# Kernel optimization log

Measured on AMD Instinct MI355X. Metric: run time of the kernel, lower is better.

Reference implementation:

```python
import jax, jax.numpy as jnp
import numpy as np

N = 50000      # nodes
E = 400000     # edges
D = 128        # node / hidden dim
DE = 64        # edge feature dim
Z = 2 * D + DE # CGConv concat dim


def setup_inputs() -> dict:
    key = jax.random.key(0)
    ks = jax.random.split(key, 12)
    s = 0.05
    return {
        "x": jax.random.normal(ks[0], (N, D), jnp.float32),
        "edge_index": jax.random.randint(ks[1], (2, E), 0, N, jnp.int64),
        "edge_attr": jax.random.normal(ks[2], (E, DE), jnp.float32),
        # conv1 params (lin_f: gate, lin_s: core), z-dim -> D
        "Wf1": jax.random.normal(ks[3], (Z, D), jnp.float32) * s,
        "bf1": jnp.zeros((D,), jnp.float32),
        "Ws1": jax.random.normal(ks[4], (Z, D), jnp.float32) * s,
        "bs1": jnp.zeros((D,), jnp.float32),
        # conv2 params
        "Wf2": jax.random.normal(ks[5], (Z, D), jnp.float32) * s,
        "bf2": jnp.zeros((D,), jnp.float32),
        "Ws2": jax.random.normal(ks[6], (Z, D), jnp.float32) * s,
        "bs2": jnp.zeros((D,), jnp.float32),
        # final linear D -> 1
        "Wfc": jax.random.normal(ks[7], (D, 1), jnp.float32) * s,
        "bfc": jnp.zeros((1,), jnp.float32),
    }


def _cgconv(h, edge_attr, src, dst, Wf, bf, Ws, bs):
    # PyG CGConv: z_ij = [x_i, x_j, e_ij]; out_i = x_i + sum_j sigmoid(lin_f(z)) * softplus(lin_s(z))
    # x_i = target = edge_index[1], x_j = source = edge_index[0]
    z = jnp.concatenate([h[dst], h[src], edge_attr], axis=-1)  # [E, Z]
    msg = jax.nn.sigmoid(z @ Wf + bf) * jax.nn.softplus(z @ Ws + bs)  # [E, D]
    agg = jax.ops.segment_sum(msg, dst, num_segments=h.shape[0])  # [N, D]
    return h + agg


def reference(x, edge_index, edge_attr, Wf1, bf1, Ws1, bs1, Wf2, bf2, Ws2, bs2, Wfc, bfc):
    src, dst = edge_index[0], edge_index[1]
    h = _cgconv(x, edge_attr, src, dst, Wf1, bf1, Ws1, bs1)
    h = jax.nn.relu(h)
    h = _cgconv(h, edge_attr, src, dst, Wf2, bf2, Ws2, bs2)
    return h @ Wfc + bfc  # [N, 1]
```

## Files before the change

### kernel.cpp

```cpp
#include <hip/hip_runtime.h>
#include <math.h>

#define NN 50000
#define NE 400000

typedef __attribute__((ext_vector_type(8))) short bf16x8;
typedef __attribute__((ext_vector_type(4))) float f32x4;
typedef unsigned short ushort_t;

__device__ __forceinline__ unsigned short f2bf(float f) {
    unsigned int u = __float_as_uint(f);
    u += 0x7FFF + ((u >> 16) & 1);
    return (unsigned short)(u >> 16);
}
__device__ __forceinline__ float2 upk(unsigned int w) {
    float2 r;
    r.x = __uint_as_float(w << 16);
    r.y = __uint_as_float(w & 0xFFFF0000u);
    return r;
}

#define LOG2E 1.4426950408889634f
#define LN2   0.6931471805599453f

__device__ __forceinline__ float msg_act(float gf, float gs) {
    float tf = __builtin_amdgcn_exp2f(gf * -LOG2E);
    float sig = __builtin_amdgcn_rcpf(1.0f + tf) * LN2;
    float ts = __builtin_amdgcn_exp2f(gs * LOG2E);
    float lg = __builtin_amdgcn_logf(1.0f + ts);
    return sig * lg;
}

__global__ void pack_weights(const float* __restrict__ Wf, const float* __restrict__ bf,
                             const float* __restrict__ Ws, const float* __restrict__ bs,
                             ushort_t* __restrict__ WT, ushort_t* __restrict__ WeT,
                             float* __restrict__ bcat) {
    int i = blockIdx.x * 256 + threadIdx.x;
    if (i < 512 * 128) {
        int c = i >> 7, k = i & 127;
        float w;
        if (c < 128)      w = Wf[k * 128 + c];
        else if (c < 256) w = Wf[(128 + k) * 128 + (c - 128)];
        else if (c < 384) w = Ws[k * 128 + (c - 256)];
        else              w = Ws[(128 + k) * 128 + (c - 384)];
        WT[i] = f2bf(w);
    } else if (i < 512 * 128 + 256 * 64) {
        int j = i - 512 * 128;
        int c = j >> 6, k = j & 63;
        float w = (c < 128) ? Wf[(256 + k) * 128 + c] : Ws[(256 + k) * 128 + (c - 128)];
        WeT[j] = f2bf(w);
    } else if (i < 512 * 128 + 256 * 64 + 256) {
        int c = i - (512 * 128 + 256 * 64);
        bcat[c] = (c < 128) ? bf[c] : bs[c - 128];
    }
}

__global__ void cvt_bf16(const float* __restrict__ in, ushort_t* __restrict__ out, int n8) {
    int i = blockIdx.x * 256 + threadIdx.x;
    if (i >= n8) return;
    const float4* p = (const float4*)in + (size_t)i * 2;
    float4 a = p[0], b = p[1];
    bf16x8 v;
    v[0] = (short)f2bf(a.x); v[1] = (short)f2bf(a.y);
    v[2] = (short)f2bf(a.z); v[3] = (short)f2bf(a.w);
    v[4] = (short)f2bf(b.x); v[5] = (short)f2bf(b.y);
    v[6] = (short)f2bf(b.z); v[7] = (short)f2bf(b.w);
    *((bf16x8*)out + i) = v;
}

__global__ __launch_bounds__(256) void node_gemm(const ushort_t* __restrict__ hb,
                                                 const ushort_t* __restrict__ WT,
                                                 ushort_t* __restrict__ P) {
    __shared__ ushort_t Bs[128 * 136];
    const int tid = threadIdx.x;
    const int w = tid >> 6, l = tid & 63;
    const int by = blockIdx.y;
    const ushort_t* src = WT + (size_t)by * 128 * 128;
    #pragma unroll
    for (int j = 0; j < 8; ++j) {
        int cid = j * 256 + tid;
        int row = cid >> 4, off = (cid & 15) * 8;
        *(bf16x8*)(&Bs[row * 136 + off]) = *(const bf16x8*)(src + row * 128 + off);
    }
    __syncthreads();
    const int r0 = blockIdx.x * 64 + w * 16;
    const int lrow = l & 15, lk = l >> 4;
    int arow = r0 + lrow;
    if (arow >= NN) arow = NN - 1;
    f32x4 acc[8];
    #pragma unroll
    for (int i = 0; i < 8; ++i) acc[i] = (f32x4){0.f, 0.f, 0.f, 0.f};
    #pragma unroll
    for (int ks = 0; ks < 4; ++ks) {
        int kb = ks * 32 + lk * 8;
        bf16x8 af = *(const bf16x8*)(hb + (size_t)arow * 128 + kb);
        #pragma unroll
        for (int nc = 0; nc < 8; ++nc) {
            bf16x8 bfr = *(const bf16x8*)(&Bs[(nc * 16 + lrow) * 136 + kb]);
            acc[nc] = __builtin_amdgcn_mfma_f32_16x16x32_bf16(af, bfr, acc[nc], 0, 0, 0);
        }
    }
    const int rb = r0 + lk * 4;
    const int cb = by * 128;
    #pragma unroll
    for (int nc = 0; nc < 8; ++nc) {
        int col = cb + nc * 16 + lrow;
        #pragma unroll
        for (int r = 0; r < 4; ++r) {
            int row = rb + r;
            if (row < NN) P[(size_t)row * 512 + col] = f2bf(acc[nc][r]);
        }
    }
}

__global__ __launch_bounds__(512) void edge_fused(const int* __restrict__ ei,
                                                  const ushort_t* __restrict__ eab,
                                                  const ushort_t* __restrict__ WeT,
                                                  const float* __restrict__ bcat,
                                                  const ushort_t* __restrict__ P,
                                                  ushort_t* __restrict__ hacc) {
    __shared__ ushort_t Qs[64 * 264];
    const int tid = threadIdx.x;
    const int w = tid >> 6, l = tid & 63;
    const int lrow = l & 15, lk = l >> 4;
    const int e0 = blockIdx.x * 64;

    const int tile = w >> 1, half = w & 1;
    f32x4 acc[8];
    #pragma unroll
    for (int i = 0; i < 8; ++i) acc[i] = (f32x4){0.f, 0.f, 0.f, 0.f};
    const int arow = e0 + tile * 16 + lrow;
    const ushort_t* wslice = WeT + (size_t)half * 128 * 64;
    #pragma unroll
    for (int ks = 0; ks < 2; ++ks) {
        int kb = ks * 32 + lk * 8;
        bf16x8 af = *(const bf16x8*)(eab + (size_t)arow * 64 + kb);
        #pragma unroll
        for (int nc = 0; nc < 8; ++nc) {
            bf16x8 bfr = *(const bf16x8*)(wslice + (size_t)(nc * 16 + lrow) * 64 + kb);
            acc[nc] = __builtin_amdgcn_mfma_f32_16x16x32_bf16(af, bfr, acc[nc], 0, 0, 0);
        }
    }
    #pragma unroll
    for (int nc = 0; nc < 8; ++nc) {
        int col = half * 128 + nc * 16 + lrow;
        float bb = bcat[col];
        #pragma unroll
        for (int r = 0; r < 4; ++r) {
            Qs[(tile * 16 + lk * 4 + r) * 264 + col] = f2bf(acc[nc][r] + bb);
        }
    }
    __syncthreads();

    #pragma unroll
    for (int i = 0; i < 8; ++i) {
        int j = w * 8 + i;
        int e = e0 + j;
        int s = ei[e];
        int d = ei[NE + e];
        const unsigned int* Pd = (const unsigned int*)(P + (size_t)d * 512);
        const unsigned int* Ps = (const unsigned int*)(P + (size_t)s * 512);
        float2 af_ = upk(Pd[l]);
        float2 bf_ = upk(Ps[64 + l]);
        float2 as_ = upk(Pd[128 + l]);
        float2 bs_ = upk(Ps[192 + l]);
        const unsigned int* qr = (const unsigned int*)(Qs + (size_t)j * 264);
        float2 qf = upk(qr[l]);
        float2 qs = upk(qr[64 + l]);
        float m0 = msg_act(af_.x + bf_.x + qf.x, as_.x + bs_.x + qs.x);
        float m1 = msg_act(af_.y + bf_.y + qf.y, as_.y + bs_.y + qs.y);
        unsigned int pk = (unsigned int)f2bf(m0) | ((unsigned int)f2bf(m1) << 16);
        unsigned int* addr = (unsigned int*)(hacc + (size_t)d * 128 + 2 * l);
        asm volatile("global_atomic_pk_add_bf16 %0, %1, off" :: "v"(addr), "v"(pk));
    }
}

__global__ void relu_bf(const ushort_t* __restrict__ in, ushort_t* __restrict__ out, int n8) {
    int i = blockIdx.x * 256 + threadIdx.x;
    if (i >= n8) return;
    uint4 v = ((const uint4*)in)[i];
    unsigned int* pv = (unsigned int*)&v;
    #pragma unroll
    for (int j = 0; j < 4; ++j) {
        unsigned int u = pv[j];
        unsigned int lo = (u & 0x8000u) ? 0u : (u & 0xFFFFu);
        unsigned int hi = (u & 0x80000000u) ? 0u : (u & 0xFFFF0000u);
        pv[j] = lo | hi;
    }
    ((uint4*)out)[i] = v;
}

__global__ __launch_bounds__(256) void final_fc(const ushort_t* __restrict__ hb,
                                                const float* __restrict__ W,
                                                const float* __restrict__ b,
                                                float* __restrict__ out) {
    int gid = blockIdx.x * 256 + threadIdx.x;
    int n = gid >> 6, lane = gid & 63;
    if (n >= NN) return;
    unsigned int hv = ((const unsigned int*)(hb + (size_t)n * 128))[lane];
    float2 h2 = upk(hv);
    float2 wv = ((const float2*)W)[lane];
    float p = h2.x * wv.x + h2.y * wv.y;
    #pragma unroll
    for (int off = 32; off > 0; off >>= 1) p += __shfl_down(p, off);
    if (lane == 0) out[n] = p + b[0];
}

extern "C" void kernel_launch(void* const* d_in, const int* in_sizes, int n_in,
                              void* d_out, int out_size, void* d_ws, size_t ws_size,
                              hipStream_t stream) {
    const float* x   = (const float*)d_in[0];
    const int*   ei  = (const int*)d_in[1];
    const float* ea  = (const float*)d_in[2];
    const float* Wf1 = (const float*)d_in[3];
    const float* bf1 = (const float*)d_in[4];
    const float* Ws1 = (const float*)d_in[5];
    const float* bs1 = (const float*)d_in[6];
    const float* Wf2 = (const float*)d_in[7];
    const float* bf2 = (const float*)d_in[8];
    const float* Ws2 = (const float*)d_in[9];
    const float* bs2 = (const float*)d_in[10];
    const float* Wfc = (const float*)d_in[11];
    const float* bfc = (const float*)d_in[12];
    float* out = (float*)d_out;

    ushort_t* hb1 = (ushort_t*)d_ws;
    ushort_t* hb2 = hb1 + (size_t)NN * 128;
    ushort_t* P   = hb2 + (size_t)NN * 128;
    ushort_t* eab = P + (size_t)NN * 512;
    ushort_t* WT  = eab + (size_t)NE * 64;
    ushort_t* WeT = WT + 2 * 512 * 128;
    float* bcat   = (float*)(WeT + 2 * 256 * 64);

    cvt_bf16<<<(NN * 128 / 8 + 255) / 256, 256, 0, stream>>>(x, hb1, NN * 128 / 8);
    cvt_bf16<<<(NE * 64 / 8 + 255) / 256, 256, 0, stream>>>(ea, eab, NE * 64 / 8);
    const int packN = 512 * 128 + 256 * 64 + 256;
    pack_weights<<<(packN + 255) / 256, 256, 0, stream>>>(Wf1, bf1, Ws1, bs1,
                                                          WT, WeT, bcat);
    pack_weights<<<(packN + 255) / 256, 256, 0, stream>>>(Wf2, bf2, Ws2, bs2,
                                                          WT + 512 * 128, WeT + 256 * 64, bcat + 256);

    for (int conv = 0; conv < 2; ++conv) {
        ushort_t* h = conv ? hb2 : hb1;
        node_gemm<<<dim3((NN + 63) / 64, 4), 256, 0, stream>>>(h, WT + conv * 512 * 128, P);
        edge_fused<<<NE / 64, 512, 0, stream>>>(ei, eab, WeT + conv * 256 * 64,
                                                bcat + conv * 256, P, h);
        if (conv == 0) {
            relu_bf<<<(NN * 128 / 8 + 255) / 256, 256, 0, stream>>>(hb1, hb2, NN * 128 / 8);
        }
    }
    final_fc<<<((size_t)NN * 64 + 255) / 256, 256, 0, stream>>>(hb2, Wfc, bfc, out);
}
```

Baseline: 400.6 us.

## Warp-specialize edge kernel so gathers overlap the edge-feature MFMA

The edge kernel is split by warp role. Four warps compute the edge-attribute GEMM into shared memory while eight other warps gather the dst and src node projections into registers at the same time; after a barrier, the gather warps apply the activation and issue the atomics. Node projections move from one 512-wide row per node to two arrays, one for dst and one for src, with the gate and core values interleaved. Each lane can then fetch both pre-activations with a single 8-byte load. Blocks now cover 32 edges with 768 threads, which adds register pressure and leaves fewer edges per block to amortize the barrier.

```diff
diff --git a/kernel.cpp b/kernel.cpp
--- a/kernel.cpp
+++ b/kernel.cpp
@@ -70,8 +70,9 @@
 
 __global__ __launch_bounds__(256) void node_gemm(const ushort_t* __restrict__ hb,
                                                  const ushort_t* __restrict__ WT,
-                                                 ushort_t* __restrict__ P) {
-    __shared__ ushort_t Bs[128 * 136];
+                                                 ushort_t* __restrict__ Pd,
+                                                 ushort_t* __restrict__ Ps) {
+    __shared__ ushort_t Bs_[128 * 136];
     const int tid = threadIdx.x;
     const int w = tid >> 6, l = tid & 63;
     const int by = blockIdx.y;
@@ -80,7 +81,7 @@
     for (int j = 0; j < 8; ++j) {
         int cid = j * 256 + tid;
         int row = cid >> 4, off = (cid & 15) * 8;
-        *(bf16x8*)(&Bs[row * 136 + off]) = *(const bf16x8*)(src + row * 128 + off);
+        *(bf16x8*)(&Bs_[row * 136 + off]) = *(const bf16x8*)(src + row * 128 + off);
     }
     __syncthreads();
     const int r0 = blockIdx.x * 64 + w * 16;
@@ -96,82 +97,96 @@
         bf16x8 af = *(const bf16x8*)(hb + (size_t)arow * 128 + kb);
         #pragma unroll
         for (int nc = 0; nc < 8; ++nc) {
-            bf16x8 bfr = *(const bf16x8*)(&Bs[(nc * 16 + lrow) * 136 + kb]);
+            bf16x8 bfr = *(const bf16x8*)(&Bs_[(nc * 16 + lrow) * 136 + kb]);
             acc[nc] = __builtin_amdgcn_mfma_f32_16x16x32_bf16(af, bfr, acc[nc], 0, 0, 0);
         }
     }
     const int rb = r0 + lk * 4;
-    const int cb = by * 128;
+    const int sel = by >> 1;
+    ushort_t* Pt = (by & 1) ? Ps : Pd;
     #pragma unroll
     for (int nc = 0; nc < 8; ++nc) {
-        int col = cb + nc * 16 + lrow;
+        int a = nc * 16 + lrow;
         #pragma unroll
         for (int r = 0; r < 4; ++r) {
             int row = rb + r;
-            if (row < NN) P[(size_t)row * 512 + col] = f2bf(acc[nc][r]);
-        }
-    }
-}
-
-__global__ __launch_bounds__(512) void edge_fused(const int* __restrict__ ei,
-                                                  const ushort_t* __restrict__ eab,
-                                                  const ushort_t* __restrict__ WeT,
-                                                  const float* __restrict__ bcat,
-                                                  const ushort_t* __restrict__ P,
-                                                  ushort_t* __restrict__ hacc) {
-    __shared__ ushort_t Qs[64 * 264];
+            if (row < NN) Pt[(size_t)row * 256 + a * 2 + sel] = f2bf(acc[nc][r]);
+        }
+    }
+}
+
+__global__ __launch_bounds__(768, 6) void edge_fused(const int* __restrict__ ei,
+                                                     const ushort_t* __restrict__ eab,
+                                                     const ushort_t* __restrict__ WeT,
+                                                     const float* __restrict__ bcat,
+                                                     const ushort_t* __restrict__ Pd,
+                                                     const ushort_t* __restrict__ Ps,
+                                                     ushort_t* __restrict__ hacc) {
+    __shared__ ushort_t Qs[32 * 260];
     const int tid = threadIdx.x;
     const int w = tid >> 6, l = tid & 63;
-    const int lrow = l & 15, lk = l >> 4;
-    const int e0 = blockIdx.x * 64;
-
-    const int tile = w >> 1, half = w & 1;
-    f32x4 acc[8];
-    #pragma unroll
-    for (int i = 0; i < 8; ++i) acc[i] = (f32x4){0.f, 0.f, 0.f, 0.f};
-    const int arow = e0 + tile * 16 + lrow;
-    const ushort_t* wslice = WeT + (size_t)half * 128 * 64;
-    #pragma unroll
-    for (int ks = 0; ks < 2; ++ks) {
-        int kb = ks * 32 + lk * 8;
-        bf16x8 af = *(const bf16x8*)(eab + (size_t)arow * 64 + kb);
+    const int e0 = blockIdx.x * 32;
+
+    int dd[4];
+    uint2 A[4], B[4];
+
+    if (w < 4) {
+        const int lrow = l & 15, lk = l >> 4;
+        const int tile = w >> 1, half = w & 1;
+        f32x4 acc[8];
+        #pragma unroll
+        for (int i = 0; i < 8; ++i) acc[i] = (f32x4){0.f, 0.f, 0.f, 0.f};
+        const int arow = e0 + tile * 16 + lrow;
+        const ushort_t* wslice = WeT + (size_t)half * 128 * 64;
+        #pragma unroll
+        for (int ks = 0; ks < 2; ++ks) {
+            int kb = ks * 32 + lk * 8;
+            bf16x8 af = *(const bf16x8*)(eab + (size_t)arow * 64 + kb);
+            #pragma unroll
+            for (int nc = 0; nc < 8; ++nc) {
+                bf16x8 bfr = *(const bf16x8*)(wslice + (size_t)(nc * 16 + lrow) * 64 + kb);
+                acc[nc] = __builtin_amdgcn_mfma_f32_16x16x32_bf16(af, bfr, acc[nc], 0, 0, 0);
+            }
+        }
         #pragma unroll
         for (int nc = 0; nc < 8; ++nc) {
-            bf16x8 bfr = *(const bf16x8*)(wslice + (size_t)(nc * 16 + lrow) * 64 + kb);
-            acc[nc] = __builtin_amdgcn_mfma_f32_16x16x32_bf16(af, bfr, acc[nc], 0, 0, 0);
-        }
-    }
-    #pragma unroll
-    for (int nc = 0; nc < 8; ++nc) {
-        int col = half * 128 + nc * 16 + lrow;
-        float bb = bcat[col];
-        #pragma unroll
-        for (int r = 0; r < 4; ++r) {
-            Qs[(tile * 16 + lk * 4 + r) * 264 + col] = f2bf(acc[nc][r] + bb);
-        }
+            int a = nc * 16 + lrow;
+            float bb = bcat[half * 128 + a];
+            #pragma unroll
+            for (int r = 0; r < 4; ++r) {
+                Qs[(tile * 16 + lk * 4 + r) * 260 + a * 2 + half] = f2bf(acc[nc][r] + bb);
+            }
+        }
+    } else {
+        const int cid = w - 4;
+        #pragma unroll
+        for (int i = 0; i < 4; ++i) {
+            int e = e0 + cid * 4 + i;
+            int s = ei[e];
+            int d = ei[NE + e];
+            dd[i] = d;
+            A[i] = ((const uint2*)(Pd + (size_t)d * 256))[l];
+            B[i] = ((const uint2*)(Ps + (size_t)s * 256))[l];
+        }
+        __builtin_amdgcn_sched_barrier(0);
     }
     __syncthreads();
 
-    #pragma unroll
-    for (int i = 0; i < 8; ++i) {
-        int j = w * 8 + i;
-        int e = e0 + j;
-        int s = ei[e];
-        int d = ei[NE + e];
-        const unsigned int* Pd = (const unsigned int*)(P + (size_t)d * 512);
-        const unsigned int* Ps = (const unsigned int*)(P + (size_t)s * 512);
-        float2 af_ = upk(Pd[l]);
-        float2 bf_ = upk(Ps[64 + l]);
-        float2 as_ = upk(Pd[128 + l]);
-        float2 bs_ = upk(Ps[192 + l]);
-        const unsigned int* qr = (const unsigned int*)(Qs + (size_t)j * 264);
-        float2 qf = upk(qr[l]);
-        float2 qs = upk(qr[64 + l]);
-        float m0 = msg_act(af_.x + bf_.x + qf.x, as_.x + bs_.x + qs.x);
-        float m1 = msg_act(af_.y + bf_.y + qf.y, as_.y + bs_.y + qs.y);
-        unsigned int pk = (unsigned int)f2bf(m0) | ((unsigned int)f2bf(m1) << 16);
-        unsigned int* addr = (unsigned int*)(hacc + (size_t)d * 128 + 2 * l);
-        asm volatile("global_atomic_pk_add_bf16 %0, %1, off" :: "v"(addr), "v"(pk));
+    if (w >= 4) {
+        const int cid = w - 4;
+        #pragma unroll
+        for (int i = 0; i < 4; ++i) {
+            int j = cid * 4 + i;
+            uint2 Q = *(const uint2*)(Qs + (size_t)j * 260 + (size_t)l * 4);
+            float2 a0 = upk(A[i].x), a1 = upk(A[i].y);
+            float2 b0 = upk(B[i].x), b1 = upk(B[i].y);
+            float2 q0 = upk(Q.x),    q1 = upk(Q.y);
+            float m0 = msg_act(a0.x + b0.x + q0.x, a0.y + b0.y + q0.y);
+            float m1 = msg_act(a1.x + b1.x + q1.x, a1.y + b1.y + q1.y);
+            unsigned int pk = (unsigned int)f2bf(m0) | ((unsigned int)f2bf(m1) << 16);
+            unsigned int* addr = (unsigned int*)(hacc + (size_t)dd[i] * 128 + 2 * l);
+            asm volatile("global_atomic_pk_add_bf16 %0, %1, off" :: "v"(addr), "v"(pk));
+        }
     }
 }
 
@@ -226,8 +241,9 @@
 
     ushort_t* hb1 = (ushort_t*)d_ws;
     ushort_t* hb2 = hb1 + (size_t)NN * 128;
-    ushort_t* P   = hb2 + (size_t)NN * 128;
-    ushort_t* eab = P + (size_t)NN * 512;
+    ushort_t* Pd  = hb2 + (size_t)NN * 128;
+    ushort_t* Ps  = Pd + (size_t)NN * 256;
+    ushort_t* eab = Ps + (size_t)NN * 256;
     ushort_t* WT  = eab + (size_t)NE * 64;
     ushort_t* WeT = WT + 2 * 512 * 128;
     float* bcat   = (float*)(WeT + 2 * 256 * 64);
@@ -242,9 +258,9 @@
 
     for (int conv = 0; conv < 2; ++conv) {
         ushort_t* h = conv ? hb2 : hb1;
-        node_gemm<<<dim3((NN + 63) / 64, 4), 256, 0, stream>>>(h, WT + conv * 512 * 128, P);
-        edge_fused<<<NE / 64, 512, 0, stream>>>(ei, eab, WeT + conv * 256 * 64,
-                                                bcat + conv * 256, P, h);
+        node_gemm<<<dim3((NN + 63) / 64, 4), 256, 0, stream>>>(h, WT + conv * 512 * 128, Pd, Ps);
+        edge_fused<<<NE / 32, 768, 0, stream>>>(ei, eab, WeT + conv * 256 * 64,
+                                                bcat + conv * 256, Pd, Ps, h);
         if (conv == 0) {
             relu_bf<<<(NN * 128 / 8 + 255) / 256, 256, 0, stream>>>(hb1, hb2, NN * 128 / 8);
         }
```

Result: slower. 510.5 us (+27.5%).
